# Performance work log

Measured on AMD Instinct MI355X. Metric: run time of the kernel, lower is better.

Reference implementation:

```python
import jax, jax.numpy as jnp
import numpy as np

SMOOTH = 1.0

def reference(probs, targets):
    B = probs.shape[0]
    m1 = probs.reshape(B, -1)
    m2 = targets.reshape(B, -1)
    # thresholded prediction and per-sample argmax ground truth (original acc branch)
    SR = m1 > 0.5
    GT = m2 == jnp.max(m2, axis=1, keepdims=True)
    corr = jnp.sum(SR == GT, axis=1).astype(jnp.float32)
    # original divides by SR.shape[0] == probs.shape[1] (per-sample first dim)
    acc = corr / jnp.float32(probs.shape[1])
    intersection = jnp.sum(m1 * m2, axis=1)
    score = 2.0 * (intersection + SMOOTH) / (jnp.sum(m1, axis=1) + jnp.sum(m2, axis=1) + SMOOTH)
    score = jnp.where(acc == 1.0, jnp.float32(1.0), score)
    return jnp.mean(1.0 - score)

def setup_inputs() -> dict:
    key = jax.random.key(0)
    k1, k2 = jax.random.split(key)
    probs = jax.random.uniform(k1, (32, 1, 512, 512), dtype=jnp.float32)
    targets = jax.random.uniform(k2, (32, 1, 512, 512), dtype=jnp.float32)
    return {"probs": probs, "targets": targets}
```

## Files before the change

kernel.cpp:

```cpp
#include <hip/hip_runtime.h>
#include <math.h>

#define NS 32
#define NELEM 262144
#define PBLK 16
#define GRID (NS * PBLK)
#define TPB 256
#define CHUNK (NELEM / PBLK)

#define NPART (NS * PBLK)
#define OFF_S1   0
#define OFF_S2   (NPART * 1)
#define OFF_DOT  (NPART * 2)
#define OFF_MX   (NPART * 3)
#define OFF_CGT  (NPART * 4)
#define OFF_PK   (NPART * 5)

__device__ __forceinline__ void comb(float& mx, int& pk, float m2, int pk2) {
    const bool g = m2 > mx;
    const bool e = m2 == mx;
    pk = g ? pk2 : (pk + (e ? pk2 : 0));
    mx = fmaxf(mx, m2);
}

__global__ __launch_bounds__(TPB) void k_partial(const float* __restrict__ probs,
                                                 const float* __restrict__ tgts,
                                                 float* __restrict__ wsf,
                                                 int* __restrict__ wsi) {
    const int b = blockIdx.x;
    const int s = b >> 4;
    const int c = b & (PBLK - 1);
    const size_t base = (size_t)s * NELEM + (size_t)c * CHUNK;
    const float4* __restrict__ p4 = (const float4*)(probs + base);
    const float4* __restrict__ t4 = (const float4*)(tgts + base);
    const int t = threadIdx.x;

    float4 a1 = {0.f,0.f,0.f,0.f}, a2 = {0.f,0.f,0.f,0.f}, ad = {0.f,0.f,0.f,0.f};
    int cgt = 0;
    float mxr = -INFINITY;
    int pkr = 0;

#pragma unroll
    for (int g = 0; g < 4; ++g) {
        float4 pv[4], tv[4];
#pragma unroll
        for (int k = 0; k < 4; ++k) {
            const int idx = g * 1024 + k * 256 + t;
            pv[k] = p4[idx];
            tv[k] = t4[idx];
        }

#pragma unroll
        for (int k = 0; k < 4; ++k) {
            a1.x += pv[k].x; a1.y += pv[k].y; a1.z += pv[k].z; a1.w += pv[k].w;
            a2.x += tv[k].x; a2.y += tv[k].y; a2.z += tv[k].z; a2.w += tv[k].w;
            ad.x = fmaf(pv[k].x, tv[k].x, ad.x);
            ad.y = fmaf(pv[k].y, tv[k].y, ad.y);
            ad.z = fmaf(pv[k].z, tv[k].z, ad.z);
            ad.w = fmaf(pv[k].w, tv[k].w, ad.w);
        }

        float4 mm;
        mm.x = fmaxf(fmaxf(tv[0].x, tv[1].x), fmaxf(tv[2].x, tv[3].x));
        mm.y = fmaxf(fmaxf(tv[0].y, tv[1].y), fmaxf(tv[2].y, tv[3].y));
        mm.z = fmaxf(fmaxf(tv[0].z, tv[1].z), fmaxf(tv[2].z, tv[3].z));
        mm.w = fmaxf(fmaxf(tv[0].w, tv[1].w), fmaxf(tv[2].w, tv[3].w));
        const float mg = fmaxf(fmaxf(mm.x, mm.y), fmaxf(mm.z, mm.w));

        int cp = 0, cg = 0, gg = 0;
#pragma unroll
        for (int k = 0; k < 4; ++k) {
            const float pc[4] = {pv[k].x, pv[k].y, pv[k].z, pv[k].w};
            const float tc[4] = {tv[k].x, tv[k].y, tv[k].z, tv[k].w};
#pragma unroll
            for (int j = 0; j < 4; ++j) {
                const int b1 = pc[j] > 0.5f;
                const int eq = tc[j] == mg;
                cp += b1;
                cg += eq;
                gg += eq & b1;
            }
        }
        cgt += cp;
        comb(mxr, pkr, mg, (cg << 16) | gg);
    }

    float s1 = (a1.x + a1.y) + (a1.z + a1.w);
    float s2 = (a2.x + a2.y) + (a2.z + a2.w);
    float dt = (ad.x + ad.y) + (ad.z + ad.w);

#pragma unroll
    for (int off = 32; off; off >>= 1) {
        s1  += __shfl_xor(s1, off);
        s2  += __shfl_xor(s2, off);
        dt  += __shfl_xor(dt, off);
        cgt += __shfl_xor(cgt, off);
        const float m2 = __shfl_xor(mxr, off);
        const int  pk2 = __shfl_xor(pkr, off);
        comb(mxr, pkr, m2, pk2);
    }

    __shared__ float ls1[4], ls2[4], ldt[4], lmx[4];
    __shared__ int   lcg[4], lpk[4];
    const int w = t >> 6, lane = t & 63;
    if (lane == 0) {
        ls1[w] = s1; ls2[w] = s2; ldt[w] = dt; lmx[w] = mxr;
        lcg[w] = cgt; lpk[w] = pkr;
    }
    __syncthreads();
    if (t == 0) {
#pragma unroll
        for (int w2 = 1; w2 < TPB / 64; ++w2) {
            s1 += ls1[w2]; s2 += ls2[w2]; dt += ldt[w2]; cgt += lcg[w2];
            comb(mxr, pkr, lmx[w2], lpk[w2]);
        }
        wsf[OFF_S1  + b] = s1;
        wsf[OFF_S2  + b] = s2;
        wsf[OFF_DOT + b] = dt;
        wsf[OFF_MX  + b] = mxr;
        wsi[OFF_CGT + b] = cgt;
        wsi[OFF_PK  + b] = pkr;
    }
}

__device__ __forceinline__ void combine_max(float& mx, int& cnt, int& gt,
                                            float mx2, int cnt2, int gt2) {
    if (mx2 > mx) { mx = mx2; cnt = cnt2; gt = gt2; }
    else if (mx2 == mx) { cnt += cnt2; gt += gt2; }
}

__global__ __launch_bounds__(512) void k_final(const float* __restrict__ wsf,
                                               const int* __restrict__ wsi,
                                               float* __restrict__ out) {
    __shared__ float scores[NS];
    const int t = threadIdx.x;
    const int w = t >> 6, lane = t & 63;
    const int samp = (w << 2) + (lane >> 4);
    const int pidx = lane & 15;
    const int idx = samp * PBLK + pidx;

    float s1  = wsf[OFF_S1  + idx];
    float s2  = wsf[OFF_S2  + idx];
    float dot = wsf[OFF_DOT + idx];
    float mx  = wsf[OFF_MX  + idx];
    int   cgt = wsi[OFF_CGT + idx];
    const int pk = wsi[OFF_PK + idx];
    int   cnt = pk >> 16;
    int   gt  = pk & 0xFFFF;

#pragma unroll
    for (int off = 8; off; off >>= 1) {
        s1  += __shfl_xor(s1, off);
        s2  += __shfl_xor(s2, off);
        dot += __shfl_xor(dot, off);
        cgt += __shfl_xor(cgt, off);
        float m2 = __shfl_xor(mx, off);
        int   c2 = __shfl_xor(cnt, off);
        int   g2 = __shfl_xor(gt, off);
        combine_max(mx, cnt, gt, m2, c2, g2);
    }

    if (pidx == 0) {
        const int cle = NELEM - cgt;
        const long long corr = (long long)cle - (long long)cnt + 2LL * (long long)gt;
        float score = 2.0f * (dot + 1.0f) / (s1 + s2 + 1.0f);
        if (corr == 1) score = 1.0f;
        scores[samp] = 1.0f - score;
    }

    __syncthreads();
    if (t < 64) {
        float v = (t < NS) ? scores[t] : 0.0f;
#pragma unroll
        for (int off = 32; off; off >>= 1) v += __shfl_xor(v, off);
        if (t == 0) out[0] = v * (1.0f / (float)NS);
    }
}

extern "C" void kernel_launch(void* const* d_in, const int* in_sizes, int n_in,
                              void* d_out, int out_size, void* d_ws, size_t ws_size,
                              hipStream_t stream) {
    const float* probs = (const float*)d_in[0];
    const float* tgts  = (const float*)d_in[1];
    float* wsf = (float*)d_ws;
    int*   wsi = (int*)d_ws;
    float* out = (float*)d_out;

    k_partial<<<GRID, TPB, 0, stream>>>(probs, tgts, wsf, wsi);
    k_final<<<1, 512, 0, stream>>>(wsf, wsi, out);
}
```

Measured before the change: 19.26 us.

## Split reduction across more blocks with DPP wave reductions and a three-kernel tail

The partial kernel now defaults to 2048 blocks that each handle one pass, with per-wave results written out directly. This drops the LDS and __syncthreads block reduction and replaces shuffles with DPP row_ror and permlane swaps. A per-sample kernel and a tiny mean kernel replace the single final kernel. The goal is more memory-level parallelism and occupancy for the streaming read, at the cost of an extra kernel launch and more workspace traffic.

```diff
diff --git a/kernel.cpp b/kernel.cpp
--- a/kernel.cpp
+++ b/kernel.cpp
@@ -3,18 +3,10 @@
 
 #define NS 32
 #define NELEM 262144
-#define PBLK 16
-#define GRID (NS * PBLK)
 #define TPB 256
-#define CHUNK (NELEM / PBLK)
-
-#define NPART (NS * PBLK)
-#define OFF_S1   0
-#define OFF_S2   (NPART * 1)
-#define OFF_DOT  (NPART * 2)
-#define OFF_MX   (NPART * 3)
-#define OFF_CGT  (NPART * 4)
-#define OFF_PK   (NPART * 5)
+
+__device__ __forceinline__ unsigned f2u(float x) { return __builtin_bit_cast(unsigned, x); }
+__device__ __forceinline__ float u2f(unsigned x) { return __builtin_bit_cast(float, x); }
 
 __device__ __forceinline__ void comb(float& mx, int& pk, float m2, int pk2) {
     const bool g = m2 > mx;
@@ -23,33 +15,87 @@
     mx = fmaxf(mx, m2);
 }
 
-__global__ __launch_bounds__(TPB) void k_partial(const float* __restrict__ probs,
-                                                 const float* __restrict__ tgts,
-                                                 float* __restrict__ wsf,
-                                                 int* __restrict__ wsi) {
+template<int CTRL>
+__device__ __forceinline__ float dppf(float v) {
+    return u2f((unsigned)__builtin_amdgcn_update_dpp((int)f2u(v), (int)f2u(v),
+                                                     CTRL, 0xF, 0xF, false));
+}
+template<int CTRL>
+__device__ __forceinline__ int dppi(int v) {
+    return __builtin_amdgcn_update_dpp(v, v, CTRL, 0xF, 0xF, false);
+}
+
+template<int N>
+__device__ __forceinline__ void level_ror(float& s1, float& s2, float& dt,
+                                          int& cgt, float& mx, int& pk) {
+    s1 += dppf<0x120 + N>(s1);
+    s2 += dppf<0x120 + N>(s2);
+    dt += dppf<0x120 + N>(dt);
+    cgt += dppi<0x120 + N>(cgt);
+    const float m2 = dppf<0x120 + N>(mx);
+    const int   p2 = dppi<0x120 + N>(pk);
+    comb(mx, pk, m2, p2);
+}
+
+#if __has_builtin(__builtin_amdgcn_permlane16_swap) && __has_builtin(__builtin_amdgcn_permlane32_swap)
+template<bool WIDE>
+__device__ __forceinline__ void level_swap(float& s1, float& s2, float& dt,
+                                           int& cgt, float& mx, int& pk) {
+#define SWAP_(x) (WIDE ? __builtin_amdgcn_permlane32_swap((x), (x), false, false) \
+                       : __builtin_amdgcn_permlane16_swap((x), (x), false, false))
+    { auto r = SWAP_(f2u(s1)); s1 = u2f(r[0]) + u2f(r[1]); }
+    { auto r = SWAP_(f2u(s2)); s2 = u2f(r[0]) + u2f(r[1]); }
+    { auto r = SWAP_(f2u(dt)); dt = u2f(r[0]) + u2f(r[1]); }
+    { auto r = SWAP_((unsigned)cgt); cgt = (int)(r[0] + r[1]); }
+    { auto rm = SWAP_(f2u(mx));
+      auto rp = SWAP_((unsigned)pk);
+      float mA = u2f(rm[0]); int pA = (int)rp[0];
+      comb(mA, pA, u2f(rm[1]), (int)rp[1]);
+      mx = mA; pk = pA; }
+#undef SWAP_
+}
+#else
+template<bool WIDE>
+__device__ __forceinline__ void level_swap(float& s1, float& s2, float& dt,
+                                           int& cgt, float& mx, int& pk) {
+    const int off = WIDE ? 32 : 16;
+    s1 += __shfl_xor(s1, off);
+    s2 += __shfl_xor(s2, off);
+    dt += __shfl_xor(dt, off);
+    cgt += __shfl_xor(cgt, off);
+    const float m2 = __shfl_xor(mx, off);
+    const int   p2 = __shfl_xor(pk, off);
+    comb(mx, pk, m2, p2);
+}
+#endif
+
+template<int PASSES, int MINW>
+__global__ __launch_bounds__(TPB, MINW) void k_partial(const float* __restrict__ probs,
+                                                       const float* __restrict__ tgts,
+                                                       float* __restrict__ wsf,
+                                                       int* __restrict__ wsi,
+                                                       int nsets) {
+    constexpr int BPS = NELEM / (PASSES * TPB * 16);
     const int b = blockIdx.x;
-    const int s = b >> 4;
-    const int c = b & (PBLK - 1);
-    const size_t base = (size_t)s * NELEM + (size_t)c * CHUNK;
+    const int s = b / BPS;
+    const int c = b % BPS;
+    const size_t base = (size_t)s * NELEM + (size_t)c * (PASSES * TPB * 16);
     const float4* __restrict__ p4 = (const float4*)(probs + base);
     const float4* __restrict__ t4 = (const float4*)(tgts + base);
     const int t = threadIdx.x;
 
     float4 a1 = {0.f,0.f,0.f,0.f}, a2 = {0.f,0.f,0.f,0.f}, ad = {0.f,0.f,0.f,0.f};
-    int cgt = 0;
-    float mxr = -INFINITY;
-    int pkr = 0;
-
-#pragma unroll
-    for (int g = 0; g < 4; ++g) {
+    int cgt = 0, pk = 0;
+    float mx = -INFINITY;
+
+#pragma unroll
+    for (int g = 0; g < PASSES; ++g) {
         float4 pv[4], tv[4];
 #pragma unroll
         for (int k = 0; k < 4; ++k) {
-            const int idx = g * 1024 + k * 256 + t;
-            pv[k] = p4[idx];
-            tv[k] = t4[idx];
-        }
-
+            pv[k] = p4[g * 1024 + k * 256 + t];
+            tv[k] = t4[g * 1024 + k * 256 + t];
+        }
 #pragma unroll
         for (int k = 0; k < 4; ++k) {
             a1.x += pv[k].x; a1.y += pv[k].y; a1.z += pv[k].z; a1.w += pv[k].w;
@@ -59,14 +105,11 @@
             ad.z = fmaf(pv[k].z, tv[k].z, ad.z);
             ad.w = fmaf(pv[k].w, tv[k].w, ad.w);
         }
-
-        float4 mm;
-        mm.x = fmaxf(fmaxf(tv[0].x, tv[1].x), fmaxf(tv[2].x, tv[3].x));
-        mm.y = fmaxf(fmaxf(tv[0].y, tv[1].y), fmaxf(tv[2].y, tv[3].y));
-        mm.z = fmaxf(fmaxf(tv[0].z, tv[1].z), fmaxf(tv[2].z, tv[3].z));
-        mm.w = fmaxf(fmaxf(tv[0].w, tv[1].w), fmaxf(tv[2].w, tv[3].w));
-        const float mg = fmaxf(fmaxf(mm.x, mm.y), fmaxf(mm.z, mm.w));
-
+        const float mX = fmaxf(fmaxf(tv[0].x, tv[1].x), fmaxf(tv[2].x, tv[3].x));
+        const float mY = fmaxf(fmaxf(tv[0].y, tv[1].y), fmaxf(tv[2].y, tv[3].y));
+        const float mZ = fmaxf(fmaxf(tv[0].z, tv[1].z), fmaxf(tv[2].z, tv[3].z));
+        const float mW = fmaxf(fmaxf(tv[0].w, tv[1].w), fmaxf(tv[2].w, tv[3].w));
+        const float mg = fmaxf(fmaxf(mX, mY), fmaxf(mZ, mW));
         int cp = 0, cg = 0, gg = 0;
 #pragma unroll
         for (int k = 0; k < 4; ++k) {
@@ -82,12 +125,54 @@
             }
         }
         cgt += cp;
-        comb(mxr, pkr, mg, (cg << 16) | gg);
+        comb(mx, pk, mg, (cg << 16) | gg);
     }
 
     float s1 = (a1.x + a1.y) + (a1.z + a1.w);
     float s2 = (a2.x + a2.y) + (a2.z + a2.w);
     float dt = (ad.x + ad.y) + (ad.z + ad.w);
+
+    level_ror<8>(s1, s2, dt, cgt, mx, pk);
+    level_ror<4>(s1, s2, dt, cgt, mx, pk);
+    level_ror<2>(s1, s2, dt, cgt, mx, pk);
+    level_ror<1>(s1, s2, dt, cgt, mx, pk);
+    level_swap<false>(s1, s2, dt, cgt, mx, pk);
+    level_swap<true >(s1, s2, dt, cgt, mx, pk);
+
+    if ((t & 63) == 0) {
+        const int g = b * (TPB / 64) + (t >> 6);
+        wsf[0 * nsets + g] = s1;
+        wsf[1 * nsets + g] = s2;
+        wsf[2 * nsets + g] = dt;
+        wsf[3 * nsets + g] = mx;
+        wsi[4 * nsets + g] = cgt;
+        wsi[5 * nsets + g] = pk;
+    }
+}
+
+__device__ __forceinline__ void combine_max(float& mx, int& cnt, int& gt,
+                                            float mx2, int cnt2, int gt2) {
+    if (mx2 > mx) { mx = mx2; cnt = cnt2; gt = gt2; }
+    else if (mx2 == mx) { cnt += cnt2; gt += gt2; }
+}
+
+template<int SPS>
+__global__ __launch_bounds__(SPS) void k_sample(const float* __restrict__ wsf,
+                                                const int* __restrict__ wsi,
+                                                float* __restrict__ scores,
+                                                int nsets) {
+    const int s = blockIdx.x;
+    const int t = threadIdx.x;
+    const int idx = s * SPS + t;
+
+    float s1 = wsf[0 * nsets + idx];
+    float s2 = wsf[1 * nsets + idx];
+    float dt = wsf[2 * nsets + idx];
+    float mx = wsf[3 * nsets + idx];
+    int  cgt = wsi[4 * nsets + idx];
+    const int pk = wsi[5 * nsets + idx];
+    int cnt = pk >> 16;
+    int gt  = pk & 0xFFFF;
 
 #pragma unroll
     for (int off = 32; off; off >>= 1) {
@@ -95,86 +180,46 @@
         s2  += __shfl_xor(s2, off);
         dt  += __shfl_xor(dt, off);
         cgt += __shfl_xor(cgt, off);
-        const float m2 = __shfl_xor(mxr, off);
-        const int  pk2 = __shfl_xor(pkr, off);
-        comb(mxr, pkr, m2, pk2);
-    }
-
-    __shared__ float ls1[4], ls2[4], ldt[4], lmx[4];
-    __shared__ int   lcg[4], lpk[4];
-    const int w = t >> 6, lane = t & 63;
-    if (lane == 0) {
-        ls1[w] = s1; ls2[w] = s2; ldt[w] = dt; lmx[w] = mxr;
-        lcg[w] = cgt; lpk[w] = pkr;
-    }
-    __syncthreads();
-    if (t == 0) {
-#pragma unroll
-        for (int w2 = 1; w2 < TPB / 64; ++w2) {
-            s1 += ls1[w2]; s2 += ls2[w2]; dt += ldt[w2]; cgt += lcg[w2];
-            comb(mxr, pkr, lmx[w2], lpk[w2]);
-        }
-        wsf[OFF_S1  + b] = s1;
-        wsf[OFF_S2  + b] = s2;
-        wsf[OFF_DOT + b] = dt;
-        wsf[OFF_MX  + b] = mxr;
-        wsi[OFF_CGT + b] = cgt;
-        wsi[OFF_PK  + b] = pkr;
-    }
-}
-
-__device__ __forceinline__ void combine_max(float& mx, int& cnt, int& gt,
-                                            float mx2, int cnt2, int gt2) {
-    if (mx2 > mx) { mx = mx2; cnt = cnt2; gt = gt2; }
-    else if (mx2 == mx) { cnt += cnt2; gt += gt2; }
-}
-
-__global__ __launch_bounds__(512) void k_final(const float* __restrict__ wsf,
-                                               const int* __restrict__ wsi,
-                                               float* __restrict__ out) {
-    __shared__ float scores[NS];
-    const int t = threadIdx.x;
-    const int w = t >> 6, lane = t & 63;
-    const int samp = (w << 2) + (lane >> 4);
-    const int pidx = lane & 15;
-    const int idx = samp * PBLK + pidx;
-
-    float s1  = wsf[OFF_S1  + idx];
-    float s2  = wsf[OFF_S2  + idx];
-    float dot = wsf[OFF_DOT + idx];
-    float mx  = wsf[OFF_MX  + idx];
-    int   cgt = wsi[OFF_CGT + idx];
-    const int pk = wsi[OFF_PK + idx];
-    int   cnt = pk >> 16;
-    int   gt  = pk & 0xFFFF;
-
-#pragma unroll
-    for (int off = 8; off; off >>= 1) {
-        s1  += __shfl_xor(s1, off);
-        s2  += __shfl_xor(s2, off);
-        dot += __shfl_xor(dot, off);
-        cgt += __shfl_xor(cgt, off);
         float m2 = __shfl_xor(mx, off);
         int   c2 = __shfl_xor(cnt, off);
         int   g2 = __shfl_xor(gt, off);
         combine_max(mx, cnt, gt, m2, c2, g2);
     }
 
-    if (pidx == 0) {
+    if constexpr (SPS > 64) {
+        __shared__ float ls1[SPS / 64], ls2[SPS / 64], ldt[SPS / 64], lmx[SPS / 64];
+        __shared__ int   lcg[SPS / 64], lcn[SPS / 64], lgt[SPS / 64];
+        const int w = t >> 6;
+        if ((t & 63) == 0) {
+            ls1[w] = s1; ls2[w] = s2; ldt[w] = dt; lmx[w] = mx;
+            lcg[w] = cgt; lcn[w] = cnt; lgt[w] = gt;
+        }
+        __syncthreads();
+        if (t == 0) {
+#pragma unroll
+            for (int w2 = 1; w2 < SPS / 64; ++w2) {
+                s1 += ls1[w2]; s2 += ls2[w2]; dt += ldt[w2]; cgt += lcg[w2];
+                combine_max(mx, cnt, gt, lmx[w2], lcn[w2], lgt[w2]);
+            }
+        }
+    }
+
+    if (t == 0) {
         const int cle = NELEM - cgt;
         const long long corr = (long long)cle - (long long)cnt + 2LL * (long long)gt;
-        float score = 2.0f * (dot + 1.0f) / (s1 + s2 + 1.0f);
+        float score = 2.0f * (dt + 1.0f) / (s1 + s2 + 1.0f);
         if (corr == 1) score = 1.0f;
-        scores[samp] = 1.0f - score;
-    }
-
-    __syncthreads();
-    if (t < 64) {
-        float v = (t < NS) ? scores[t] : 0.0f;
-#pragma unroll
-        for (int off = 32; off; off >>= 1) v += __shfl_xor(v, off);
-        if (t == 0) out[0] = v * (1.0f / (float)NS);
-    }
+        scores[s] = 1.0f - score;
+    }
+}
+
+__global__ __launch_bounds__(64) void k_mean(const float* __restrict__ scores,
+                                             float* __restrict__ out) {
+    const int t = threadIdx.x;
+    float v = (t < NS) ? scores[t] : 0.0f;
+#pragma unroll
+    for (int off = 32; off; off >>= 1) v += __shfl_xor(v, off);
+    if (t == 0) out[0] = v * (1.0f / (float)NS);
 }
 
 extern "C" void kernel_launch(void* const* d_in, const int* in_sizes, int n_in,
@@ -186,6 +231,16 @@
     int*   wsi = (int*)d_ws;
     float* out = (float*)d_out;
 
-    k_partial<<<GRID, TPB, 0, stream>>>(probs, tgts, wsf, wsi);
-    k_final<<<1, 512, 0, stream>>>(wsf, wsi, out);
-}
+    const size_t need_big = (size_t)(6 * 8192 + NS) * sizeof(float);
+    if (ws_size >= need_big) {
+        const int nsets = 8192;
+        k_partial<1, 8><<<2048, TPB, 0, stream>>>(probs, tgts, wsf, wsi, nsets);
+        k_sample<256><<<NS, 256, 0, stream>>>(wsf, wsi, wsf + 6 * nsets, nsets);
+        k_mean<<<1, 64, 0, stream>>>(wsf + 6 * nsets, out);
+    } else {
+        const int nsets = 2048;
+        k_partial<4, 4><<<512, TPB, 0, stream>>>(probs, tgts, wsf, wsi, nsets);
+        k_sample<64><<<NS, 64, 0, stream>>>(wsf, wsi, wsf + 6 * nsets, nsets);
+        k_mean<<<1, 64, 0, stream>>>(wsf + 6 * nsets, out);
+    }
+}
```

New measurement: 20.13 us. 4.5% more time.
